# Performance work log

Measured on AMD Instinct MI355X. Metric: run time of the kernel, lower is better.

## Reference

```python
import jax, jax.numpy as jnp
import numpy as np

D_MODEL = 1024
N_HEADS = 16
NUM_PATTERN = 32
HEAD_DIM = D_MODEL // N_HEADS  # d_keys = d_values = 64


def sparsemax(z):
    # z: [..., S]; Euclidean projection of z onto the probability simplex
    S = z.shape[-1]
    z_sorted = -jnp.sort(-z, axis=-1)                       # descending
    cum = jnp.cumsum(z_sorted, axis=-1)
    k = jnp.arange(1, S + 1, dtype=z.dtype)
    support = (1.0 + k * z_sorted) > cum                    # [..., S] bool
    k_sup = jnp.sum(support, axis=-1, keepdims=True)        # int, size of support
    cum_sel = jnp.take_along_axis(cum, k_sup - 1, axis=-1)
    tau = (cum_sel - 1.0) / k_sup.astype(z.dtype)
    return jnp.maximum(z - tau, 0.0)


def setup_inputs() -> dict:
    key = jax.random.key(0)
    ks = jax.random.split(key, 10)
    s = 1.0 / np.sqrt(D_MODEL)
    inp = {
        "query": jax.random.normal(ks[0], (8, 4096, D_MODEL), dtype=jnp.float32),
        "key_param": jax.random.normal(ks[1], (1, NUM_PATTERN, D_MODEL), dtype=jnp.float32),
        "Wq": jax.random.normal(ks[2], (D_MODEL, N_HEADS * HEAD_DIM), dtype=jnp.float32) * s,
        "bq": jnp.zeros((N_HEADS * HEAD_DIM,), dtype=jnp.float32),
        "Wk": jax.random.normal(ks[3], (D_MODEL, N_HEADS * HEAD_DIM), dtype=jnp.float32) * s,
        "bk": jnp.zeros((N_HEADS * HEAD_DIM,), dtype=jnp.float32),
        "Wv": jax.random.normal(ks[4], (N_HEADS * HEAD_DIM, N_HEADS * HEAD_DIM), dtype=jnp.float32) * s,
        "bv": jnp.zeros((N_HEADS * HEAD_DIM,), dtype=jnp.float32),
        "Wo": jax.random.normal(ks[5], (N_HEADS * HEAD_DIM, D_MODEL), dtype=jnp.float32) * s,
        "bo": jnp.zeros((D_MODEL,), dtype=jnp.float32),
    }
    return inp


def reference(query, key_param, Wq, bq, Wk, bk, Wv, bv, Wo, bo):
    B, L, _ = query.shape
    S = key_param.shape[1]
    H, E = N_HEADS, HEAD_DIM
    D = HEAD_DIM

    k = jnp.broadcast_to(key_param, (B, S, D_MODEL))         # repeat over batch
    queries = (query @ Wq + bq).reshape(B, L, H, E)
    keys_flat = k @ Wk + bk                                  # [B, S, H*E]
    values = (keys_flat @ Wv + bv).reshape(B, S, H, D)
    keys = keys_flat.reshape(B, S, H, E)

    scale = 1.0 / np.sqrt(E)
    scores = jnp.einsum("blhe,bshe->bhls", queries, keys)    # [B, H, L, S]
    A = sparsemax(scale * scores)                            # sparse normalization over S
    out = jnp.einsum("bhls,bshd->blhd", A, values)           # [B, L, H, D]

    # mix=True: transpose(2,1) then view(B, L, -1) on contiguous data
    out = jnp.transpose(out, (0, 2, 1, 3)).reshape(B, L, H * D)
    return out @ Wo + bo
```

## Files before the change

kernel.cpp:

```cpp
#include <hip/hip_runtime.h>

typedef unsigned short u16;
typedef __attribute__((ext_vector_type(8))) short short8;
typedef __attribute__((ext_vector_type(4))) float v4f;

__device__ __forceinline__ float b2f(u16 u) {
  union { unsigned int i; float f; } v; v.i = ((unsigned int)u) << 16; return v.f;
}
__device__ __forceinline__ u16 f2b(float f) {
  unsigned int x = __float_as_uint(f);
  x += 0x7fffu + ((x >> 16) & 1u);
  return (u16)(x >> 16);
}
__device__ __forceinline__ float ldin(const void* p, size_t i, int f32) {
  return f32 ? ((const float*)p)[i] : b2f(((const u16*)p)[i]);
}

#define LDSW 40

__global__ void sniff_k(const void* __restrict__ q, int* __restrict__ flag) {
  __shared__ int cnt;
  if (threadIdx.x == 0) cnt = 0;
  __syncthreads();
  const u16* p = (const u16*)q;
  int w = 0;
  for (int i = threadIdx.x; i < 1024; i += 256) {
    u16 u = p[i];
    int e = (u >> 7) & 0xFF;
    if (u != 0 && u != 0x8000 && (e >= 0xC0 || e < 0x40)) w++;
  }
  atomicAdd(&cnt, w);
  __syncthreads();
  if (threadIdx.x == 0) *flag = (cnt >= 32) ? 1 : 0;
}

__global__ void kv_zero(float* __restrict__ Kf, float* __restrict__ Vf) {
  int i = blockIdx.x * 256 + threadIdx.x;
  Kf[i] = 0.f;
  Vf[i] = 0.f;
}

__global__ void gemm_skinny_atomic(const void* __restrict__ A, const void* __restrict__ W,
                                   const void* __restrict__ bias, float* __restrict__ C,
                                   const int* __restrict__ flag, int a_f32_always) {
  const int f32 = *flag;
  const int af = a_f32_always ? 1 : f32;
  const int t = blockIdx.x * 256 + threadIdx.x;
  const int kb = blockIdx.y;
  const int s = t >> 10, j = t & 1023;
  const int d0 = kb * 128;
  float acc = 0.f;
#pragma unroll 16
  for (int d = d0; d < d0 + 128; ++d)
    acc += ldin(A, (size_t)s * 1024 + d, af) * ldin(W, (size_t)d * 1024 + j, f32);
  if (kb == 0) acc += ldin(bias, j, f32);
  atomicAdd(&C[t], acc);
}

__global__ void kernel_K(const void* __restrict__ kp, const void* __restrict__ Wk,
                         const void* __restrict__ bk, float* __restrict__ Kf,
                         const int* __restrict__ flag) {
  const int f32 = *flag;
  int t = blockIdx.x * 256 + threadIdx.x;
  int s = t >> 10, j = t & 1023;
  float acc = 0.f;
#pragma unroll 8
  for (int d = 0; d < 1024; ++d)
    acc += ldin(kp, (size_t)s * 1024 + d, f32) * ldin(Wk, (size_t)d * 1024 + j, f32);
  Kf[t] = acc + ldin(bk, j, f32);
}

__global__ void kernel_V(const float* __restrict__ Kf, const void* __restrict__ Wv,
                         const void* __restrict__ bv, float* __restrict__ Vf,
                         const int* __restrict__ flag) {
  const int f32 = *flag;
  int t = blockIdx.x * 256 + threadIdx.x;
  int s = t >> 10, j = t & 1023;
  const float* kr = Kf + (size_t)s * 1024;
  float acc = 0.f;
#pragma unroll 8
  for (int d = 0; d < 1024; ++d) acc += kr[d] * ldin(Wv, (size_t)d * 1024 + j, f32);
  Vf[t] = acc + ldin(bv, j, f32);
}

__global__ void __launch_bounds__(256) kernel_M2(
    const float* __restrict__ Kf, const void* __restrict__ Wq,
    const void* __restrict__ bq, u16* __restrict__ Mt,
    float* __restrict__ bias_s, const int* __restrict__ flag) {
  const int f32 = *flag;
  const int blk = blockIdx.x;
  const int h = blk >> 4, dg = blk & 15;
  const int t = threadIdx.x;
  const int d = dg * 64 + (t & 63);
  const int sb = (t >> 6) * 8;
  __shared__ float ks2[64][32];
  for (int i = t; i < 2048; i += 256) {
    int s = i & 31, e = i >> 5;
    ks2[e][s] = Kf[(size_t)s * 1024 + h * 64 + e] * 0.125f;
  }
  __syncthreads();
  v4f a0 = {0.f, 0.f, 0.f, 0.f}, a1 = {0.f, 0.f, 0.f, 0.f};
  const size_t base = (size_t)d * 1024 + h * 64;
  for (int e0 = 0; e0 < 64; e0 += 8) {
    float wq[8];
    if (f32) {
      const float* W = (const float*)Wq;
      v4f v0 = *(const v4f*)(W + base + e0);
      v4f v1 = *(const v4f*)(W + base + e0 + 4);
#pragma unroll
      for (int q = 0; q < 4; ++q) { wq[q] = v0[q]; wq[4 + q] = v1[q]; }
    } else {
      const u16* W = (const u16*)Wq;
      union { uint4 v; u16 w[8]; } tv __attribute__((aligned(16)));
      tv.v = *(const uint4*)(W + base + e0);
#pragma unroll
      for (int q = 0; q < 8; ++q) wq[q] = b2f(tv.w[q]);
    }
#pragma unroll
    for (int e = 0; e < 8; ++e) {
      float w = wq[e];
      v4f k0 = *(const v4f*)&ks2[e0 + e][sb];
      v4f k1 = *(const v4f*)&ks2[e0 + e][sb + 4];
      a0 += w * k0;
      a1 += w * k1;
    }
  }
#pragma unroll
  for (int r = 0; r < 4; ++r) {
    Mt[(size_t)(h * 32 + sb + r) * 1024 + d]     = f2b(a0[r]);
    Mt[(size_t)(h * 32 + sb + 4 + r) * 1024 + d] = f2b(a1[r]);
  }
  if (dg == 0 && t < 32) {
    float a = 0.f;
    for (int e = 0; e < 64; ++e) a += ldin(bq, h * 64 + e, f32) * ks2[e][t];
    bias_s[h * 32 + t] = a;
  }
}

__global__ void kernel_N2(const float* __restrict__ Vf, const void* __restrict__ Wo,
                          u16* __restrict__ N2t, const int* __restrict__ flag) {
  const int f32 = *flag;
  int blk = blockIdx.x;
  int h = blk >> 6, r = (blk >> 2) & 15, jb = blk & 3;
  int tid = threadIdx.x;
  int j = jb * 256 + tid;
  __shared__ float vsl[2048];
  for (int i = tid; i < 2048; i += 256) {
    int s = i >> 6, d = i & 63;
    vsl[i] = Vf[(size_t)s * 1024 + h * 64 + d];
  }
  __syncthreads();
  float acc[32];
#pragma unroll
  for (int s = 0; s < 32; ++s) acc[s] = 0.f;
  for (int d = 0; d < 64; ++d) {
    float w = ldin(Wo, (size_t)(r * 64 + d) * 1024 + j, f32);
#pragma unroll
    for (int s = 0; s < 32; ++s) acc[s] += vsl[s * 64 + d] * w;
  }
  union { u16 o[32]; uint4 v[4]; } ou __attribute__((aligned(16)));
#pragma unroll
  for (int s = 0; s < 32; ++s) ou.o[s] = f2b(acc[s]);
  uint4* dst = (uint4*)(N2t + ((size_t)(h * 1024 + j)) * 512 + r * 32);
#pragma unroll
  for (int i = 0; i < 4; ++i) dst[i] = ou.v[i];
}

__global__ void kernel_bo(const void* __restrict__ bo, float* __restrict__ bo_f,
                          const int* __restrict__ flag) {
  const int f32 = *flag;
  int i = blockIdx.x * 256 + threadIdx.x;
  if (i < 1024) bo_f[i] = ldin(bo, i, f32);
}

__global__ void __launch_bounds__(512, 1) gemm_scores_wide(
    const void* __restrict__ A, const u16* __restrict__ B,
    const float* __restrict__ bias, u16* __restrict__ Z2,
    const int* __restrict__ flag) {
  const int f32 = *flag;
  const int K = 1024;
  __shared__ u16 As[128 * LDSW] __attribute__((aligned(16)));
  __shared__ u16 Bs[512 * LDSW] __attribute__((aligned(16)));
  const int tid = threadIdx.x;
  const int wave = tid >> 6;
  const int lane = tid & 63;
  const int quad = lane >> 4;
  const int l16 = lane & 15;
  const int m0 = blockIdx.x * 128;
  const int wm = (wave >> 2) * 64;
  const int wn = (wave & 3) * 128;

  v4f acc[4][8] = {};

  const int ra = tid >> 2, ca = (tid & 3) * 8;

  for (int k0 = 0; k0 < K; k0 += 32) {
    size_t offA = (size_t)(m0 + ra) * K + k0 + ca;
    if (!f32) {
      *(uint4*)&As[ra * LDSW + ca] = *(const uint4*)((const u16*)A + offA);
    } else {
      const float* fA = (const float*)A;
      v4f a0 = *(const v4f*)(fA + offA);
      v4f a1 = *(const v4f*)(fA + offA + 4);
      union { uint4 v; u16 w[8]; } t0 __attribute__((aligned(16)));
#pragma unroll
      for (int e = 0; e < 4; ++e) { t0.w[e] = f2b(a0[e]); t0.w[e + 4] = f2b(a1[e]); }
      *(uint4*)&As[ra * LDSW + ca] = t0.v;
    }
#pragma unroll
    for (int p = 0; p < 4; ++p) {
      int idx = tid + p * 512;
      int rb = idx >> 2, cb = (idx & 3) * 8;
      *(uint4*)&Bs[rb * LDSW + cb] = *(const uint4*)(B + (size_t)rb * K + k0 + cb);
    }
    __syncthreads();
    short8 af[4], bf[8];
#pragma unroll
    for (int i = 0; i < 4; ++i)
      af[i] = *(const short8*)&As[(wm + i * 16 + l16) * LDSW + quad * 8];
#pragma unroll
    for (int i = 0; i < 8; ++i)
      bf[i] = *(const short8*)&Bs[(wn + i * 16 + l16) * LDSW + quad * 8];
#pragma unroll
    for (int mi = 0; mi < 4; ++mi)
#pragma unroll
      for (int ni = 0; ni < 8; ++ni)
        acc[mi][ni] = __builtin_amdgcn_mfma_f32_16x16x32_bf16(af[mi], bf[ni], acc[mi][ni], 0, 0, 0);
    __syncthreads();
  }

#pragma unroll
  for (int ni = 0; ni < 8; ++ni) {
    const int col = wn + ni * 16 + l16;
    const float bcol = bias[col];
    const int h = col >> 5, s = col & 31;
#pragma unroll
    for (int mi = 0; mi < 4; ++mi) {
      const int rbase = m0 + wm + mi * 16 + quad * 4;
#pragma unroll
      for (int rr = 0; rr < 4; ++rr) {
        const int rw = rbase + rr;
        const size_t addr = (size_t)h * 1048576 + (size_t)(rw >> 4) * 512 + (rw & 15) * 32 + s;
        Z2[addr] = f2b(acc[mi][ni][rr] + bcol);
      }
    }
  }
}

__global__ void sparsemax_k(u16* __restrict__ Z) {
  int t = blockIdx.x * 256 + threadIdx.x;
  u16* zp = Z + (size_t)t * 32;
  union { uint4 v[4]; u16 w[32]; } raw __attribute__((aligned(16)));
  const uint4* rp4 = (const uint4*)zp;
#pragma unroll
  for (int i = 0; i < 4; ++i) raw.v[i] = rp4[i];
  float z[32], zs[32];
#pragma unroll
  for (int i = 0; i < 32; ++i) { z[i] = b2f(raw.w[i]); zs[i] = z[i]; }
#pragma unroll
  for (int kk = 2; kk <= 32; kk <<= 1) {
#pragma unroll
    for (int j = kk >> 1; j > 0; j >>= 1) {
#pragma unroll
      for (int i = 0; i < 32; ++i) {
        int ij = i ^ j;
        if (ij > i) {
          bool up = ((i & kk) == 0);
          float a = zs[i], b = zs[ij];
          float hi = fmaxf(a, b), lo = fminf(a, b);
          zs[i]  = up ? hi : lo;
          zs[ij] = up ? lo : hi;
        }
      }
    }
  }
  float cum = 0.f, cumsel = 0.f;
  int ksup = 1;
#pragma unroll
  for (int i = 0; i < 32; ++i) {
    cum += zs[i];
    if (1.f + (float)(i + 1) * zs[i] > cum) { ksup = i + 1; cumsel = cum; }
  }
  float tau = (cumsel - 1.f) / (float)ksup;
  union { u16 o[32]; uint4 v[4]; } ou __attribute__((aligned(16)));
#pragma unroll
  for (int i = 0; i < 32; ++i) ou.o[i] = f2b(fmaxf(z[i] - tau, 0.f));
  uint4* op = (uint4*)zp;
#pragma unroll
  for (int i = 0; i < 4; ++i) op[i] = ou.v[i];
}

__global__ void __launch_bounds__(512, 1) gemm_out_wide(
    const u16* __restrict__ Z2, const u16* __restrict__ N2t,
    const float* __restrict__ bias, void* __restrict__ out,
    const int* __restrict__ flag) {
  const int f32 = *flag;
  const int K = 512;
  const int h = blockIdx.z;
  __shared__ u16 As[128 * LDSW] __attribute__((aligned(16)));
  __shared__ u16 Bs[512 * LDSW] __attribute__((aligned(16)));
  const int tid = threadIdx.x;
  const int wave = tid >> 6;
  const int lane = tid & 63;
  const int quad = lane >> 4;
  const int l16 = lane & 15;
  const int m0 = blockIdx.y * 128;
  const int n0 = blockIdx.x * 512;
  const int wm = (wave >> 2) * 64;
  const int wn = (wave & 3) * 128;

  v4f acc[4][8] = {};

  const u16* Ab = Z2 + (size_t)h * 2048 * 512 + (size_t)m0 * K;
  const u16* Bb = N2t + (size_t)h * 1024 * 512 + (size_t)n0 * K;
  const int ra = tid >> 2, ca = (tid & 3) * 8;

  for (int k0 = 0; k0 < K; k0 += 32) {
    *(uint4*)&As[ra * LDSW + ca] = *(const uint4*)(Ab + (size_t)ra * K + k0 + ca);
#pragma unroll
    for (int p = 0; p < 4; ++p) {
      int idx = tid + p * 512;
      int rb = idx >> 2, cb = (idx & 3) * 8;
      *(uint4*)&Bs[rb * LDSW + cb] = *(const uint4*)(Bb + (size_t)rb * K + k0 + cb);
    }
    __syncthreads();
    short8 af[4], bf[8];
#pragma unroll
    for (int i = 0; i < 4; ++i)
      af[i] = *(const short8*)&As[(wm + i * 16 + l16) * LDSW + quad * 8];
#pragma unroll
    for (int i = 0; i < 8; ++i)
      bf[i] = *(const short8*)&Bs[(wn + i * 16 + l16) * LDSW + quad * 8];
#pragma unroll
    for (int mi = 0; mi < 4; ++mi)
#pragma unroll
      for (int ni = 0; ni < 8; ++ni)
        acc[mi][ni] = __builtin_amdgcn_mfma_f32_16x16x32_bf16(af[mi], bf[ni], acc[mi][ni], 0, 0, 0);
    __syncthreads();
  }

  float bv8[8];
#pragma unroll
  for (int ni = 0; ni < 8; ++ni) bv8[ni] = bias[n0 + wn + ni * 16 + l16];
#pragma unroll
  for (int mi = 0; mi < 4; ++mi) {
    const int rl = m0 + wm + mi * 16 + quad * 4;
#pragma unroll
    for (int rr = 0; rr < 4; ++rr) {
      const int rlr = rl + rr;
      const int orow = (rlr >> 8) * 4096 + h * 256 + (rlr & 255);
#pragma unroll
      for (int ni = 0; ni < 8; ++ni) {
        const int col = n0 + wn + ni * 16 + l16;
        const float v = acc[mi][ni][rr] + bv8[ni];
        const size_t oi = (size_t)orow * 1024 + col;
        if (f32) ((float*)out)[oi] = v;
        else     ((u16*)out)[oi] = f2b(v);
      }
    }
  }
}

__global__ void __launch_bounds__(256) fused_fallback(
    const void* __restrict__ query, const u16* __restrict__ Mt,
    const float* __restrict__ bias_s, const u16* __restrict__ N2t,
    const float* __restrict__ bo_f, void* __restrict__ out,
    const int* __restrict__ flag) {
  const int f32 = *flag;
  __shared__ float sc[256 * 32];
  __shared__ u16 qch[256 * 72];
  __shared__ u16 mh[32 * 64];
  const int t = threadIdx.x;
  const int bb = blockIdx.x;
  const int b = bb >> 4, atile = bb & 15;
  const int l0 = atile * 256;
  const size_t qbase = ((size_t)b * 4096 + l0) * 1024;

  for (int h = 0; h < 16; ++h) {
    float acc32[32];
#pragma unroll
    for (int s = 0; s < 32; ++s) acc32[s] = bias_s[h * 32 + s];
    for (int d0 = 0; d0 < 1024; d0 += 64) {
      __syncthreads();
#pragma unroll
      for (int i = 0; i < 8; ++i) {
        int f4 = t + i * 256;
        int row = f4 >> 3, c8 = f4 & 7;
        size_t off = qbase + (size_t)row * 1024 + d0 + c8 * 8;
        if (!f32) {
          *(uint4*)&qch[row * 72 + c8 * 8] = *(const uint4*)((const u16*)query + off);
        } else {
          union { uint4 v; u16 w[8]; } tq __attribute__((aligned(16)));
#pragma unroll
          for (int e = 0; e < 8; ++e) tq.w[e] = f2b(((const float*)query)[off + e]);
          *(uint4*)&qch[row * 72 + c8 * 8] = tq.v;
        }
      }
      { int row = t >> 3, c8 = t & 7;
        *(uint4*)&mh[row * 64 + c8 * 8] =
            *(const uint4*)(Mt + (size_t)(h * 32 + row) * 1024 + d0 + c8 * 8); }
      __syncthreads();
      float qrow[64];
#pragma unroll
      for (int c = 0; c < 64; ++c) qrow[c] = b2f(qch[t * 72 + c]);
#pragma unroll 4
      for (int s = 0; s < 32; ++s) {
        float a = 0.f;
#pragma unroll
        for (int c = 0; c < 64; ++c) a += qrow[c] * b2f(mh[s * 64 + c]);
        acc32[s] += a;
      }
    }
    float zs[32];
#pragma unroll
    for (int i = 0; i < 32; ++i) zs[i] = acc32[i];
#pragma unroll
    for (int kk = 2; kk <= 32; kk <<= 1) {
#pragma unroll
      for (int j = kk >> 1; j > 0; j >>= 1) {
#pragma unroll
        for (int i = 0; i < 32; ++i) {
          int ij = i ^ j;
          if (ij > i) {
            bool up = ((i & kk) == 0);
            float a = zs[i], bq_ = zs[ij];
            float hi = fmaxf(a, bq_), lo = fminf(a, bq_);
            zs[i]  = up ? hi : lo;
            zs[ij] = up ? lo : hi;
          }
        }
      }
    }
    float cum = 0.f, cumsel = 0.f;
    int ksup = 1;
#pragma unroll
    for (int i = 0; i < 32; ++i) {
      cum += zs[i];
      if (1.f + (float)(i + 1) * zs[i] > cum) { ksup = i + 1; cumsel = cum; }
    }
    float tau = (cumsel - 1.f) / (float)ksup;
#pragma unroll
    for (int s = 0; s < 32; ++s) sc[t * 32 + s] = fmaxf(acc32[s] - tau, 0.f);
    __syncthreads();
    for (int jj = 0; jj < 4; ++jj) {
      int j = t + jj * 256;
      const u16* nrow = N2t + ((size_t)h * 1024 + j) * 512;
      float acc16[16];
#pragma unroll
      for (int a = 0; a < 16; ++a) acc16[a] = 0.f;
      for (int k0 = 0; k0 < 512; k0 += 8) {
        union { uint4 v; u16 w[8]; } nv __attribute__((aligned(16)));
        nv.v = *(const uint4*)(nrow + k0);
#pragma unroll
        for (int kk = 0; kk < 8; ++kk) {
          float nf = b2f(nv.w[kk]);
#pragma unroll
          for (int a = 0; a < 16; ++a) acc16[a] += sc[a * 512 + k0 + kk] * nf;
        }
      }
      float bj = bo_f[j];
#pragma unroll
      for (int a = 0; a < 16; ++a) {
        int orow = b * 4096 + h * 256 + atile * 16 + a;
        size_t oi = (size_t)orow * 1024 + j;
        float v = acc16[a] + bj;
        if (f32) ((float*)out)[oi] = v;
        else     ((u16*)out)[oi] = f2b(v);
      }
    }
    __syncthreads();
  }
}

__global__ void zero_out(void* __restrict__ out, int n, const int* __restrict__ flag) {
  const int f32 = *flag;
  int i = blockIdx.x * 256 + threadIdx.x;
  if (i < n) { if (f32) ((float*)out)[i] = 0.f; else ((u16*)out)[i] = 0; }
}

extern "C" void kernel_launch(void* const* d_in, const int* in_sizes, int n_in,
                              void* d_out, int out_size, void* d_ws, size_t ws_size,
                              hipStream_t stream) {
  const void* query = d_in[0];
  const void* kp    = d_in[1];
  const void* Wq    = d_in[2];
  const void* bq    = d_in[3];
  const void* Wk    = d_in[4];
  const void* bk    = d_in[5];
  const void* Wv    = d_in[6];
  const void* bv    = d_in[7];
  const void* Wo    = d_in[8];
  const void* bo    = d_in[9];

  char* ws = (char*)d_ws;
  int*   flag   = (int*)(ws);
  float* Kf     = (float*)(ws + (64 << 10));
  float* Vf     = (float*)(ws + (192 << 10));
  float* bias_s = (float*)(ws + (320 << 10));
  float* bo_f   = (float*)(ws + (324 << 10));
  u16*   Mt     = (u16*)(ws + (1 << 20));
  u16*   N2t    = (u16*)(ws + (2 << 20));
  u16*   Z2     = (u16*)(ws + (18 << 20));

  const size_t WS_FAST = (size_t)(18 << 20) + 33554432;
  const size_t WS_FALL = (size_t)(18 << 20);

  sniff_k<<<1, 256, 0, stream>>>(query, flag);

  if (ws_size >= WS_FAST) {
    kv_zero<<<128, 256, 0, stream>>>(Kf, Vf);
    gemm_skinny_atomic<<<dim3(128, 8), 256, 0, stream>>>(kp, Wk, bk, Kf, flag, 0);
    gemm_skinny_atomic<<<dim3(128, 8), 256, 0, stream>>>(Kf, Wv, bv, Vf, flag, 1);
    kernel_M2<<<256, 256, 0, stream>>>(Kf, Wq, bq, Mt, bias_s, flag);
    kernel_N2<<<1024, 256, 0, stream>>>(Vf, Wo, N2t, flag);
    kernel_bo<<<4, 256, 0, stream>>>(bo, bo_f, flag);
    gemm_scores_wide<<<256, 512, 0, stream>>>(query, Mt, bias_s, Z2, flag);
    sparsemax_k<<<2048, 256, 0, stream>>>(Z2);
    gemm_out_wide<<<dim3(2, 16, 16), 512, 0, stream>>>(Z2, N2t, bo_f, d_out, flag);
  } else if (ws_size >= WS_FALL) {
    kernel_K<<<128, 256, 0, stream>>>(kp, Wk, bk, Kf, flag);
    kernel_V<<<128, 256, 0, stream>>>(Kf, Wv, bv, Vf, flag);
    kernel_M2<<<256, 256, 0, stream>>>(Kf, Wq, bq, Mt, bias_s, flag);
    kernel_N2<<<1024, 256, 0, stream>>>(Vf, Wo, N2t, flag);
    kernel_bo<<<4, 256, 0, stream>>>(bo, bo_f, flag);
    fused_fallback<<<128, 256, 0, stream>>>(query, Mt, bias_s, N2t, bo_f, d_out, flag);
  } else {
    zero_out<<<(out_size + 255) / 256, 256, 0, stream>>>(d_out, out_size, flag);
  }
}
```

Baseline: 451.1 us.

## Double-buffer LDS tiles with register prefetch in score and output GEMMs

Both wide MFMA GEMM kernels now use two LDS buffers. The global loads for tile t+2 are staged in registers while tile t is computed, so global-memory latency overlaps MFMA work instead of stalling before each k-step. Each kernel's LDS use doubles to about 100KB per block. That is acceptable at one block per CU, but it adds register pressure from the prefetch registers and keeps two barriers per iteration.

```diff
diff --git a/kernel.cpp b/kernel.cpp
--- a/kernel.cpp
+++ b/kernel.cpp
@@ -179,8 +179,9 @@
     const int* __restrict__ flag) {
   const int f32 = *flag;
   const int K = 1024;
-  __shared__ u16 As[128 * LDSW] __attribute__((aligned(16)));
-  __shared__ u16 Bs[512 * LDSW] __attribute__((aligned(16)));
+  const int NT = 32;
+  __shared__ u16 As[2][128 * LDSW] __attribute__((aligned(16)));
+  __shared__ u16 Bs[2][512 * LDSW] __attribute__((aligned(16)));
   const int tid = threadIdx.x;
   const int wave = tid >> 6;
   const int lane = tid & 63;
@@ -193,41 +194,72 @@
   v4f acc[4][8] = {};
 
   const int ra = tid >> 2, ca = (tid & 3) * 8;
-
-  for (int k0 = 0; k0 < K; k0 += 32) {
-    size_t offA = (size_t)(m0 + ra) * K + k0 + ca;
-    if (!f32) {
-      *(uint4*)&As[ra * LDSW + ca] = *(const uint4*)((const u16*)A + offA);
-    } else {
-      const float* fA = (const float*)A;
-      v4f a0 = *(const v4f*)(fA + offA);
-      v4f a1 = *(const v4f*)(fA + offA + 4);
-      union { uint4 v; u16 w[8]; } t0 __attribute__((aligned(16)));
-#pragma unroll
-      for (int e = 0; e < 4; ++e) { t0.w[e] = f2b(a0[e]); t0.w[e + 4] = f2b(a1[e]); }
-      *(uint4*)&As[ra * LDSW + ca] = t0.v;
-    }
-#pragma unroll
-    for (int p = 0; p < 4; ++p) {
-      int idx = tid + p * 512;
-      int rb = idx >> 2, cb = (idx & 3) * 8;
-      *(uint4*)&Bs[rb * LDSW + cb] = *(const uint4*)(B + (size_t)rb * K + k0 + cb);
-    }
-    __syncthreads();
+  v4f raf0, raf1;
+  uint4 rau;
+  uint4 rb_[4];
+
+#define S_LOAD(t_) do {                                                        \
+    size_t offA = (size_t)(m0 + ra) * K + (size_t)(t_) * 32 + ca;              \
+    if (f32) {                                                                 \
+      const float* fA = (const float*)A;                                       \
+      raf0 = *(const v4f*)(fA + offA);                                         \
+      raf1 = *(const v4f*)(fA + offA + 4);                                     \
+    } else {                                                                   \
+      rau = *(const uint4*)((const u16*)A + offA);                             \
+    }                                                                          \
+    _Pragma("unroll")                                                          \
+    for (int p = 0; p < 4; ++p) {                                              \
+      int idx = tid + p * 512;                                                 \
+      int rb = idx >> 2, cb = (idx & 3) * 8;                                   \
+      rb_[p] = *(const uint4*)(B + (size_t)rb * K + (size_t)(t_) * 32 + cb);   \
+    }                                                                          \
+  } while (0)
+
+#define S_WRITE(buf) do {                                                      \
+    if (f32) {                                                                 \
+      union { uint4 v; u16 w[8]; } t0 __attribute__((aligned(16)));            \
+      _Pragma("unroll")                                                        \
+      for (int e = 0; e < 4; ++e) { t0.w[e] = f2b(raf0[e]); t0.w[e + 4] = f2b(raf1[e]); } \
+      *(uint4*)&As[buf][ra * LDSW + ca] = t0.v;                                \
+    } else {                                                                   \
+      *(uint4*)&As[buf][ra * LDSW + ca] = rau;                                 \
+    }                                                                          \
+    _Pragma("unroll")                                                          \
+    for (int p = 0; p < 4; ++p) {                                              \
+      int idx = tid + p * 512;                                                 \
+      int rb = idx >> 2, cb = (idx & 3) * 8;                                   \
+      *(uint4*)&Bs[buf][rb * LDSW + cb] = rb_[p];                              \
+    }                                                                          \
+  } while (0)
+
+  S_LOAD(0);
+  S_WRITE(0);
+  S_LOAD(1);
+  __syncthreads();
+
+  for (int t = 0; t < NT; ++t) {
+    const int cur = t & 1;
     short8 af[4], bf[8];
 #pragma unroll
     for (int i = 0; i < 4; ++i)
-      af[i] = *(const short8*)&As[(wm + i * 16 + l16) * LDSW + quad * 8];
+      af[i] = *(const short8*)&As[cur][(wm + i * 16 + l16) * LDSW + quad * 8];
 #pragma unroll
     for (int i = 0; i < 8; ++i)
-      bf[i] = *(const short8*)&Bs[(wn + i * 16 + l16) * LDSW + quad * 8];
+      bf[i] = *(const short8*)&Bs[cur][(wn + i * 16 + l16) * LDSW + quad * 8];
 #pragma unroll
     for (int mi = 0; mi < 4; ++mi)
 #pragma unroll
       for (int ni = 0; ni < 8; ++ni)
         acc[mi][ni] = __builtin_amdgcn_mfma_f32_16x16x32_bf16(af[mi], bf[ni], acc[mi][ni], 0, 0, 0);
-    __syncthreads();
-  }
+    if (t < NT - 1) {
+      __syncthreads();
+      S_WRITE(cur ^ 1);
+      if (t < NT - 2) S_LOAD(t + 2);
+      __syncthreads();
+    }
+  }
+#undef S_LOAD
+#undef S_WRITE
 
 #pragma unroll
   for (int ni = 0; ni < 8; ++ni) {
@@ -296,9 +328,10 @@
     const int* __restrict__ flag) {
   const int f32 = *flag;
   const int K = 512;
+  const int NT = 16;
   const int h = blockIdx.z;
-  __shared__ u16 As[128 * LDSW] __attribute__((aligned(16)));
-  __shared__ u16 Bs[512 * LDSW] __attribute__((aligned(16)));
+  __shared__ u16 As[2][128 * LDSW] __attribute__((aligned(16)));
+  __shared__ u16 Bs[2][512 * LDSW] __attribute__((aligned(16)));
   const int tid = threadIdx.x;
   const int wave = tid >> 6;
   const int lane = tid & 63;
@@ -314,30 +347,57 @@
   const u16* Ab = Z2 + (size_t)h * 2048 * 512 + (size_t)m0 * K;
   const u16* Bb = N2t + (size_t)h * 1024 * 512 + (size_t)n0 * K;
   const int ra = tid >> 2, ca = (tid & 3) * 8;
-
-  for (int k0 = 0; k0 < K; k0 += 32) {
-    *(uint4*)&As[ra * LDSW + ca] = *(const uint4*)(Ab + (size_t)ra * K + k0 + ca);
-#pragma unroll
-    for (int p = 0; p < 4; ++p) {
-      int idx = tid + p * 512;
-      int rb = idx >> 2, cb = (idx & 3) * 8;
-      *(uint4*)&Bs[rb * LDSW + cb] = *(const uint4*)(Bb + (size_t)rb * K + k0 + cb);
-    }
-    __syncthreads();
+  uint4 rau;
+  uint4 rb_[4];
+
+#define S_LOAD(t_) do {                                                        \
+    rau = *(const uint4*)(Ab + (size_t)ra * K + (size_t)(t_) * 32 + ca);       \
+    _Pragma("unroll")                                                          \
+    for (int p = 0; p < 4; ++p) {                                              \
+      int idx = tid + p * 512;                                                 \
+      int rb = idx >> 2, cb = (idx & 3) * 8;                                   \
+      rb_[p] = *(const uint4*)(Bb + (size_t)rb * K + (size_t)(t_) * 32 + cb);  \
+    }                                                                          \
+  } while (0)
+
+#define S_WRITE(buf) do {                                                      \
+    *(uint4*)&As[buf][ra * LDSW + ca] = rau;                                   \
+    _Pragma("unroll")                                                          \
+    for (int p = 0; p < 4; ++p) {                                              \
+      int idx = tid + p * 512;                                                 \
+      int rb = idx >> 2, cb = (idx & 3) * 8;                                   \
+      *(uint4*)&Bs[buf][rb * LDSW + cb] = rb_[p];                              \
+    }                                                                          \
+  } while (0)
+
+  S_LOAD(0);
+  S_WRITE(0);
+  S_LOAD(1);
+  __syncthreads();
+
+  for (int t = 0; t < NT; ++t) {
+    const int cur = t & 1;
     short8 af[4], bf[8];
 #pragma unroll
     for (int i = 0; i < 4; ++i)
-      af[i] = *(const short8*)&As[(wm + i * 16 + l16) * LDSW + quad * 8];
+      af[i] = *(const short8*)&As[cur][(wm + i * 16 + l16) * LDSW + quad * 8];
 #pragma unroll
     for (int i = 0; i < 8; ++i)
-      bf[i] = *(const short8*)&Bs[(wn + i * 16 + l16) * LDSW + quad * 8];
+      bf[i] = *(const short8*)&Bs[cur][(wn + i * 16 + l16) * LDSW + quad * 8];
 #pragma unroll
     for (int mi = 0; mi < 4; ++mi)
 #pragma unroll
       for (int ni = 0; ni < 8; ++ni)
         acc[mi][ni] = __builtin_amdgcn_mfma_f32_16x16x32_bf16(af[mi], bf[ni], acc[mi][ni], 0, 0, 0);
-    __syncthreads();
-  }
+    if (t < NT - 1) {
+      __syncthreads();
+      S_WRITE(cur ^ 1);
+      if (t < NT - 2) S_LOAD(t + 2);
+      __syncthreads();
+    }
+  }
+#undef S_LOAD
+#undef S_WRITE
 
   float bv8[8];
 #pragma unroll
```

Result: slower. 492.5 us (+9.2%).
